# Kernel tuning notes

Measured on AMD Instinct MI355X. Metric: run time of the kernel, lower is better.

## Reference

```python
import jax, jax.numpy as jnp
import numpy as np

C0, C1, C2 = 2000, 10000, 50000  # class cutoffs
D = 1024                          # input_size (hidden dim)
OUT_HEAD = C0 + 2                 # head output: shortlist + 2 cluster logits


def setup_inputs() -> dict:
    key = jax.random.key(0)
    ks = jax.random.split(key, 7)
    s = lambda fan_in: 1.0 / np.sqrt(fan_in)
    x = jax.random.normal(ks[0], (4096, D), dtype=jnp.float32)
    Wh = jax.random.normal(ks[1], (OUT_HEAD, D), dtype=jnp.float32) * s(D)
    bh = jnp.zeros((OUT_HEAD,), dtype=jnp.float32)
    # tail 0: D -> D//4**0 -> (C1-C0)
    W0a = jax.random.normal(ks[2], (D, D), dtype=jnp.float32) * s(D)
    W0b = jax.random.normal(ks[3], (C1 - C0, D), dtype=jnp.float32) * s(D)
    # tail 1: D -> D//4**1 -> (C2-C1)
    W1a = jax.random.normal(ks[4], (D // 4, D), dtype=jnp.float32) * s(D)
    W1b = jax.random.normal(ks[5], (C2 - C1, D // 4), dtype=jnp.float32) * s(D // 4)
    return {"x": x, "Wh": Wh, "bh": bh, "W0a": W0a, "W0b": W0b, "W1a": W1a, "W1b": W1b}


def reference(x, Wh, bh, W0a, W0b, W1a, W1b):
    # head: [B, OUT_HEAD]; log-softmax over shortlist + cluster logits
    lsm_head = jax.nn.log_softmax(x @ Wh.T + bh, axis=-1)
    # tail clusters: capacity-reduction linear, projection, log-softmax within cluster
    lsm_t0 = jax.nn.log_softmax((x @ W0a.T) @ W0b.T, axis=-1)  # [B, C1-C0]
    lsm_t1 = jax.nn.log_softmax((x @ W1a.T) @ W1b.T, axis=-1)  # [B, C2-C1]
    # flat log-probs: cluster log-prob broadcast-added to within-cluster log-probs
    prob = jnp.concatenate([
        lsm_head[:, :C0],
        lsm_head[:, C0:C0 + 1] + lsm_t0,
        lsm_head[:, C0 + 1:C0 + 2] + lsm_t1,
    ], axis=1)  # [B, C2]
    return prob
```

## Files before the change

kernel.cpp:

```cpp
#include <hip/hip_runtime.h>
#include <hip/hip_bf16.h>
#include <math.h>

#define CC0 2000
#define CC1 10000
#define CC2 50000
#define DH  1024
#define BATCH 4096
#define OUT_HEAD (CC0 + 2)

typedef __attribute__((ext_vector_type(4))) float  f32x4;
typedef __attribute__((ext_vector_type(8))) __bf16 bf16x8;
typedef __attribute__((ext_vector_type(8))) short  s16x8;

__device__ __forceinline__ void gload_lds16(const void* g, void* l) {
    __builtin_amdgcn_global_load_lds(
        (const __attribute__((address_space(1))) void*)g,
        (__attribute__((address_space(3))) void*)l, 16, 0, 0);
}

__global__ __launch_bounds__(256) void convert_all_kernel(
    const float4* __restrict__ s0, ushort4* __restrict__ d0, int n0s, int n0d,
    const float4* __restrict__ s1, ushort4* __restrict__ d1, int n1s, int n1d,
    const float4* __restrict__ s2, ushort4* __restrict__ d2, int n2s, int n2d,
    const float4* __restrict__ s3, ushort4* __restrict__ d3, int n3s, int n3d,
    const float4* __restrict__ s4, ushort4* __restrict__ d4, int n4s, int n4d,
    const float4* __restrict__ s5, ushort4* __restrict__ d5, int n5s, int n5d,
    float* __restrict__ rs0, float* __restrict__ rs1)
{
    if (blockIdx.y == 6) {
        int i = blockIdx.x * blockDim.x + threadIdx.x;
        if (i < BATCH) { rs0[i] = 0.f; rs1[i] = 0.f; }
        return;
    }
    const float4* src; ushort4* dst; int ns, nd;
    switch (blockIdx.y) {
        case 0: src = s0; dst = d0; ns = n0s; nd = n0d; break;
        case 1: src = s1; dst = d1; ns = n1s; nd = n1d; break;
        case 2: src = s2; dst = d2; ns = n2s; nd = n2d; break;
        case 3: src = s3; dst = d3; ns = n3s; nd = n3d; break;
        case 4: src = s4; dst = d4; ns = n4s; nd = n4d; break;
        default: src = s5; dst = d5; ns = n5s; nd = n5d; break;
    }
    int i = blockIdx.x * blockDim.x + threadIdx.x;
    const int stride = gridDim.x * blockDim.x;
    for (; i < nd; i += stride) {
        ushort4 o = {0, 0, 0, 0};
        if (i < ns) {
            float4 v = src[i];
            o.x = __builtin_bit_cast(unsigned short, (__bf16)v.x);
            o.y = __builtin_bit_cast(unsigned short, (__bf16)v.y);
            o.z = __builtin_bit_cast(unsigned short, (__bf16)v.z);
            o.w = __builtin_bit_cast(unsigned short, (__bf16)v.w);
        }
        dst[i] = o;
    }
}

__global__ __launch_bounds__(256) void gemm128x3_kernel(
    const ushort* __restrict__ x_bf,
    const ushort* __restrict__ W0a_bf, ushort* __restrict__ h0,
    const ushort* __restrict__ W1a_bf, ushort* __restrict__ h1,
    const ushort* __restrict__ Wh_bf,  float*  __restrict__ headL)
{
    __shared__ ushort As[128 * 64];
    __shared__ ushort Bs[128 * 64];

    const int gb = blockIdx.x;
    const ushort* A = x_bf; const ushort* B; void* C;
    int N, ldC, wmode, nbx, lin;
    const int K = DH;
    if (gb < 256)      { B = W0a_bf; C = h0;    N = DH;       ldC = DH;       wmode = 1; nbx = 8;  lin = gb; }
    else if (gb < 320) { B = W1a_bf; C = h1;    N = 256;      ldC = 256;      wmode = 1; nbx = 2;  lin = gb - 256; }
    else               { B = Wh_bf;  C = headL; N = OUT_HEAD; ldC = OUT_HEAD; wmode = 2; nbx = 16; lin = gb - 320; }

    const int nwg = nbx * 32;
    const int q = nwg >> 3;
    int bid = (lin & 7) * q + (lin >> 3);
    const int bx = bid % nbx;
    const int by = bid / nbx;

    const int t = threadIdx.x;
    const int lane = t & 63;
    const int w = t >> 6;
    const int wr = w >> 1, wc = w & 1;
    const int lr = lane & 15;
    const int lg = lane >> 4;
    const int bm = by * 128;
    const int bn = bx * 128;
    const int lrow = lane >> 3;
    const int lcol = (lane & 7) * 8;

    f32x4 acc[4][4] = {};

    for (int k0 = 0; k0 < K; k0 += 64) {
        #pragma unroll
        for (int i = 0; i < 4; ++i) {
            const int seg = w * 4 + i;
            const int row = seg * 8 + lrow;
            gload_lds16(A + (size_t)(bm + row) * K + k0 + lcol, &As[seg * 512]);
            gload_lds16(B + (size_t)(bn + row) * K + k0 + lcol, &Bs[seg * 512]);
        }
        __syncthreads();
        #pragma unroll
        for (int ks = 0; ks < 2; ++ks) {
            s16x8 af[4], bfr[4];
            #pragma unroll
            for (int m = 0; m < 4; ++m)
                af[m] = *(const s16x8*)&As[(wr * 64 + m * 16 + lr) * 64 + ks * 32 + lg * 8];
            #pragma unroll
            for (int n = 0; n < 4; ++n)
                bfr[n] = *(const s16x8*)&Bs[(wc * 64 + n * 16 + lr) * 64 + ks * 32 + lg * 8];
            #pragma unroll
            for (int m = 0; m < 4; ++m)
                #pragma unroll
                for (int n = 0; n < 4; ++n)
                    acc[m][n] = __builtin_amdgcn_mfma_f32_16x16x32_bf16(
                        __builtin_bit_cast(bf16x8, af[m]),
                        __builtin_bit_cast(bf16x8, bfr[n]), acc[m][n], 0, 0, 0);
        }
        __syncthreads();
    }

    #pragma unroll
    for (int m = 0; m < 4; ++m) {
        #pragma unroll
        for (int r = 0; r < 4; ++r) {
            const int row = bm + wr * 64 + m * 16 + lg * 4 + r;
            #pragma unroll
            for (int n = 0; n < 4; ++n) {
                const int col = bn + wc * 64 + n * 16 + lr;
                float v = acc[m][n][r];
                if (col < N) {
                    if (wmode == 1)
                        ((ushort*)C)[(size_t)row * ldC + col] =
                            __builtin_bit_cast(unsigned short, (__bf16)v);
                    else
                        ((float*)C)[(size_t)row * ldC + col] = v;
                }
            }
        }
    }
}

template <int WMODE, bool SUMEXP>
__global__ __launch_bounds__(512, 1) void gemm256_kernel(
    const ushort* __restrict__ A, const ushort* __restrict__ B,
    void* __restrict__ Cp, int M, int N, int K, int ldC,
    float* __restrict__ rowsum, const float* __restrict__ addv)
{
    __shared__ ushort lds[2][2][256 * 64];

    const int nby = gridDim.y;
    const int nwg = gridDim.x * gridDim.y;
    const int q8 = nwg >> 3;
    int bid = blockIdx.y * gridDim.x + blockIdx.x;
    bid = (bid & 7) * q8 + (bid >> 3);
    const int by = bid % nby;
    const int bx = bid / nby;
    const int bm = by * 256, bn = bx * 256;

    const int t = threadIdx.x;
    const int lane = t & 63;
    const int w = t >> 6;
    const int wr = w >> 2;
    const int wc = w & 3;
    const int lr = lane & 15;
    const int lg = lane >> 4;
    const int xr = (lr & 7) << 4;
    const int c0 = w * 64 + lane;

    f32x4 acc[8][4] = {};
    const int nkt = K / 64;

    auto stage_tile = [&](int ktile, int buf) {
        const int k0 = ktile * 64;
        #pragma unroll
        for (int h = 0; h < 4; ++h) {
            const int r0 = (h >> 1) * 128;
            const int mat = h & 1;
            const ushort* gbase = mat ? B : A;
            const int brow = mat ? bn : bm;
            #pragma unroll
            for (int i = 0; i < 2; ++i) {
                const int c = i * 512 + c0;
                const int rl = c >> 3;
                const int cc = (c & 7) ^ (rl & 7);
                gload_lds16(gbase + (size_t)(brow + r0 + rl) * K + k0 + cc * 8,
                            (char*)&lds[buf][mat][0] + r0 * 128 + (i * 512 + w * 64) * 16);
            }
        }
    };

    stage_tile(0, 0);
    asm volatile("s_waitcnt vmcnt(0)");
    __builtin_amdgcn_s_barrier();
    asm volatile("" ::: "memory");

    for (int tk = 0; tk < nkt; ++tk) {
        const int cur = tk & 1;
        if (tk + 1 < nkt) stage_tile(tk + 1, cur ^ 1);
        const char* baseA = (const char*)&lds[cur][0][0];
        const char* baseB = (const char*)&lds[cur][1][0];

        s16x8 bfr[4][2];
        #pragma unroll
        for (int n_ = 0; n_ < 4; ++n_) {
            const int row = wc * 64 + n_ * 16 + lr;
            #pragma unroll
            for (int ks = 0; ks < 2; ++ks)
                bfr[n_][ks] = *(const s16x8*)(baseB + (row * 128 + ((ks * 64 + lg * 16) ^ xr)));
        }
        #pragma unroll
        for (int mh = 0; mh < 2; ++mh) {
            s16x8 af[4][2];
            #pragma unroll
            for (int m_ = 0; m_ < 4; ++m_) {
                const int row = wr * 128 + (mh * 4 + m_) * 16 + lr;
                #pragma unroll
                for (int ks = 0; ks < 2; ++ks)
                    af[m_][ks] = *(const s16x8*)(baseA + (row * 128 + ((ks * 64 + lg * 16) ^ xr)));
            }
            __builtin_amdgcn_s_setprio(1);
            #pragma unroll
            for (int m_ = 0; m_ < 4; ++m_)
                #pragma unroll
                for (int n_ = 0; n_ < 4; ++n_)
                    #pragma unroll
                    for (int ks = 0; ks < 2; ++ks)
                        acc[mh * 4 + m_][n_] = __builtin_amdgcn_mfma_f32_16x16x32_bf16(
                            __builtin_bit_cast(bf16x8, af[m_][ks]),
                            __builtin_bit_cast(bf16x8, bfr[n_][ks]),
                            acc[mh * 4 + m_][n_], 0, 0, 0);
            __builtin_amdgcn_s_setprio(0);
        }
        asm volatile("s_waitcnt vmcnt(0)" ::: "memory");
        __builtin_amdgcn_s_barrier();
        asm volatile("" ::: "memory");
    }

    #pragma unroll
    for (int m = 0; m < 8; ++m) {
        #pragma unroll
        for (int r = 0; r < 4; ++r) {
            const int row = bm + wr * 128 + m * 16 + lg * 4 + r;
            const float addr_ = (WMODE == 3) ? addv[row] : 0.f;
            float psum = 0.f;
            #pragma unroll
            for (int n = 0; n < 4; ++n) {
                const int col = bn + wc * 64 + n * 16 + lr;
                float v = acc[m][n][r];
                if (col < N) {
                    if (WMODE == 1)
                        ((ushort*)Cp)[(size_t)row * ldC + col] =
                            __builtin_bit_cast(unsigned short, (__bf16)v);
                    else if (WMODE == 3)
                        ((float*)Cp)[(size_t)row * ldC + col] = v + addr_;
                    if (SUMEXP) psum += __expf(v);
                }
            }
            if (SUMEXP) {
                #pragma unroll
                for (int mm = 1; mm < 16; mm <<= 1) psum += __shfl_xor(psum, mm, 64);
                if (lr == 0) atomicAdd(&rowsum[row], psum);
            }
        }
    }
}

__global__ __launch_bounds__(256) void head_lsm_kernel(
    const float* __restrict__ HL, const float* __restrict__ bh,
    float* __restrict__ out, float* __restrict__ s01)
{
    const int row = blockIdx.x;
    const float* L = HL + (size_t)row * OUT_HEAD;
    const int t = threadIdx.x;
    __shared__ float red[4];

    float m = -1e30f;
    for (int i = t; i < OUT_HEAD; i += 256) m = fmaxf(m, L[i] + bh[i]);
    #pragma unroll
    for (int s = 1; s < 64; s <<= 1) m = fmaxf(m, __shfl_xor(m, s, 64));
    if ((t & 63) == 0) red[t >> 6] = m;
    __syncthreads();
    m = fmaxf(fmaxf(red[0], red[1]), fmaxf(red[2], red[3]));

    float sum = 0.f;
    for (int i = t; i < OUT_HEAD; i += 256) sum += __expf(L[i] + bh[i] - m);
    #pragma unroll
    for (int s = 1; s < 64; s <<= 1) sum += __shfl_xor(sum, s, 64);
    __syncthreads();
    if ((t & 63) == 0) red[t >> 6] = sum;
    __syncthreads();
    const float lse = m + logf(red[0] + red[1] + red[2] + red[3]);

    float* orow = out + (size_t)row * CC2;
    for (int i = t; i < CC0; i += 256) orow[i] = L[i] + bh[i] - lse;
    if (t == 0) {
        s01[2 * row + 0] = L[CC0 + 0] + bh[CC0 + 0] - lse;
        s01[2 * row + 1] = L[CC0 + 1] + bh[CC0 + 1] - lse;
    }
}

__global__ __launch_bounds__(256) void prep_add_kernel(
    const float* __restrict__ s01, const float* __restrict__ rs0,
    const float* __restrict__ rs1, float* __restrict__ add0,
    float* __restrict__ add1, int n)
{
    int i = blockIdx.x * blockDim.x + threadIdx.x;
    if (i < n) {
        add0[i] = s01[2 * i + 0] - logf(rs0[i]);
        add1[i] = s01[2 * i + 1] - logf(rs1[i]);
    }
}

__global__ __launch_bounds__(256) void finalize_bf16_kernel(
    const ushort* __restrict__ Lg, int ldL, int ncols8,
    float* __restrict__ outb, const float* __restrict__ addv)
{
    const int row = blockIdx.y;
    const float add = addv[row];
    const int c = blockIdx.x * blockDim.x + threadIdx.x;
    if (c >= ncols8) return;
    s16x8 v = *(const s16x8*)(Lg + (size_t)row * ldL + c * 8);
    float* o = outb + (size_t)row * CC2 + c * 8;
    float4 o0, o1;
    o0.x = __builtin_bit_cast(float, (unsigned)(unsigned short)v[0] << 16) + add;
    o0.y = __builtin_bit_cast(float, (unsigned)(unsigned short)v[1] << 16) + add;
    o0.z = __builtin_bit_cast(float, (unsigned)(unsigned short)v[2] << 16) + add;
    o0.w = __builtin_bit_cast(float, (unsigned)(unsigned short)v[3] << 16) + add;
    o1.x = __builtin_bit_cast(float, (unsigned)(unsigned short)v[4] << 16) + add;
    o1.y = __builtin_bit_cast(float, (unsigned)(unsigned short)v[5] << 16) + add;
    o1.z = __builtin_bit_cast(float, (unsigned)(unsigned short)v[6] << 16) + add;
    o1.w = __builtin_bit_cast(float, (unsigned)(unsigned short)v[7] << 16) + add;
    *(float4*)o = o0;
    *(float4*)(o + 4) = o1;
}

extern "C" void kernel_launch(void* const* d_in, const int* in_sizes, int n_in,
                              void* d_out, int out_size, void* d_ws, size_t ws_size,
                              hipStream_t stream) {
    const float* x   = (const float*)d_in[0];
    const float* Wh  = (const float*)d_in[1];
    const float* bh  = (const float*)d_in[2];
    const float* W0a = (const float*)d_in[3];
    const float* W0b = (const float*)d_in[4];
    const float* W1a = (const float*)d_in[5];
    const float* W1b = (const float*)d_in[6];
    float* out = (float*)d_out;
    char*  ws  = (char*)d_ws;

    const int NH_P  = 2048;
    const int N0_P  = 8192;
    const int N1_P  = 40192;

    size_t off = 0;
    auto alloc = [&](size_t bytes) { size_t o = off; off += (bytes + 255) & ~(size_t)255; return o; };
    ushort* x_bf   = (ushort*)(ws + alloc((size_t)BATCH * DH * 2));
    ushort* Wh_bf  = (ushort*)(ws + alloc((size_t)NH_P * DH * 2));
    ushort* W0a_bf = (ushort*)(ws + alloc((size_t)DH * DH * 2));
    ushort* W0b_bf = (ushort*)(ws + alloc((size_t)N0_P * DH * 2));
    ushort* W1a_bf = (ushort*)(ws + alloc((size_t)256 * DH * 2));
    ushort* W1b_bf = (ushort*)(ws + alloc((size_t)N1_P * 256 * 2));
    ushort* h0_bf  = (ushort*)(ws + alloc((size_t)BATCH * DH * 2));
    ushort* h1_bf  = (ushort*)(ws + alloc((size_t)BATCH * 256 * 2));
    float*  headL  = (float*)(ws + alloc((size_t)BATCH * OUT_HEAD * 4));
    float*  s01    = (float*)(ws + alloc((size_t)BATCH * 2 * 4));
    float*  rs0    = (float*)(ws + alloc((size_t)BATCH * 4));
    float*  rs1    = (float*)(ws + alloc((size_t)BATCH * 4));
    float*  add0   = (float*)(ws + alloc((size_t)BATCH * 4));
    float*  add1   = (float*)(ws + alloc((size_t)BATCH * 4));
    ushort* L0     = (ushort*)(ws + alloc((size_t)BATCH * N0_P * 2));

    convert_all_kernel<<<dim3(1280, 7), 256, 0, stream>>>(
        (const float4*)x,   (ushort4*)x_bf,   BATCH * DH / 4,        BATCH * DH / 4,
        (const float4*)Wh,  (ushort4*)Wh_bf,  OUT_HEAD * DH / 4,     NH_P * DH / 4,
        (const float4*)W0a, (ushort4*)W0a_bf, DH * DH / 4,           DH * DH / 4,
        (const float4*)W0b, (ushort4*)W0b_bf, (CC1 - CC0) * DH / 4,  N0_P * DH / 4,
        (const float4*)W1a, (ushort4*)W1a_bf, 256 * DH / 4,          256 * DH / 4,
        (const float4*)W1b, (ushort4*)W1b_bf, (CC2 - CC1) * 256 / 4, N1_P * 256 / 4,
        rs0, rs1);

    gemm128x3_kernel<<<832, 256, 0, stream>>>(
        x_bf, W0a_bf, h0_bf, W1a_bf, h1_bf, Wh_bf, headL);

    head_lsm_kernel<<<BATCH, 256, 0, stream>>>(headL, bh, out, s01);
    gemm256_kernel<1, true><<<dim3(N0_P / 256, BATCH / 256), 512, 0, stream>>>(
        h0_bf, W0b_bf, L0, BATCH, CC1 - CC0, DH, N0_P, rs0, nullptr);
    gemm256_kernel<0, true><<<dim3(N1_P / 256, BATCH / 256), 512, 0, stream>>>(
        h1_bf, W1b_bf, nullptr, BATCH, CC2 - CC1, 256, 0, rs1, nullptr);
    prep_add_kernel<<<(BATCH + 255) / 256, 256, 0, stream>>>(s01, rs0, rs1, add0, add1, BATCH);
    gemm256_kernel<3, false><<<dim3(N1_P / 256, BATCH / 256), 512, 0, stream>>>(
        h1_bf, W1b_bf, out + CC1, BATCH, CC2 - CC1, 256, CC2, nullptr, add1);
    finalize_bf16_kernel<<<dim3((1000 + 255) / 256, BATCH), 256, 0, stream>>>(
        L0, N0_P, 1000, out + CC0, add0);
}
```

Before: 643.8 us.

## Merge tail GEMMs into one launch and store tail-1 logits instead of recomputing

Both tail projection GEMMs now run in one launch that dispatches on block index. The second cluster's logits are stored as bf16 in a new workspace buffer, so the second GEMM over W1b is no longer run again just to write output. A single finalize kernel then converts both tail buffers to fp32 and adds the per-row offsets. This removes one K=256 GEMM pass and a launch, at the cost of a round trip of about 330 MB through bf16 memory and bf16 rounding of the tail-1 output values.

```diff
diff --git a/kernel.cpp b/kernel.cpp
--- a/kernel.cpp
+++ b/kernel.cpp
@@ -8,6 +8,10 @@
 #define DH  1024
 #define BATCH 4096
 #define OUT_HEAD (CC0 + 2)
+
+#define N0_P 8192
+#define N1_P 40192
+#define NH_P 2048
 
 typedef __attribute__((ext_vector_type(4))) float  f32x4;
 typedef __attribute__((ext_vector_type(8))) __bf16 bf16x8;
@@ -67,7 +71,7 @@
     __shared__ ushort Bs[128 * 64];
 
     const int gb = blockIdx.x;
-    const ushort* A = x_bf; const ushort* B; void* C;
+    const ushort* B; void* C;
     int N, ldC, wmode, nbx, lin;
     const int K = DH;
     if (gb < 256)      { B = W0a_bf; C = h0;    N = DH;       ldC = DH;       wmode = 1; nbx = 8;  lin = gb; }
@@ -98,7 +102,7 @@
         for (int i = 0; i < 4; ++i) {
             const int seg = w * 4 + i;
             const int row = seg * 8 + lrow;
-            gload_lds16(A + (size_t)(bm + row) * K + k0 + lcol, &As[seg * 512]);
+            gload_lds16(x_bf + (size_t)(bm + row) * K + k0 + lcol, &As[seg * 512]);
             gload_lds16(B + (size_t)(bn + row) * K + k0 + lcol, &Bs[seg * 512]);
         }
         __syncthreads();
@@ -123,7 +127,7 @@
     }
 
     #pragma unroll
-    for (int m = 0; m < 4; ++m) {
+    for (int m = 0; m < 4; ++m)
         #pragma unroll
         for (int r = 0; r < 4; ++r) {
             const int row = bm + wr * 64 + m * 16 + lg * 4 + r;
@@ -140,24 +144,27 @@
                 }
             }
         }
-    }
-}
-
-template <int WMODE, bool SUMEXP>
-__global__ __launch_bounds__(512, 1) void gemm256_kernel(
-    const ushort* __restrict__ A, const ushort* __restrict__ B,
-    void* __restrict__ Cp, int M, int N, int K, int ldC,
-    float* __restrict__ rowsum, const float* __restrict__ addv)
+}
+
+__global__ __launch_bounds__(512, 1) void tails256_kernel(
+    const ushort* __restrict__ h0, const ushort* __restrict__ W0b,
+    ushort* __restrict__ L0, float* __restrict__ rs0,
+    const ushort* __restrict__ h1, const ushort* __restrict__ W1b,
+    ushort* __restrict__ L1, float* __restrict__ rs1)
 {
     __shared__ ushort lds[2][2][256 * 64];
 
-    const int nby = gridDim.y;
-    const int nwg = gridDim.x * gridDim.y;
+    const int gb = blockIdx.x;
+    const ushort *A, *B; ushort* C; float* rsum;
+    int K, N, nbx, ldC, lin;
+    if (gb < 512) { A = h0; B = W0b; C = L0; rsum = rs0; K = DH;  N = CC1 - CC0; nbx = N0_P / 256; ldC = N0_P; lin = gb; }
+    else          { A = h1; B = W1b; C = L1; rsum = rs1; K = 256; N = CC2 - CC1; nbx = N1_P / 256; ldC = N1_P; lin = gb - 512; }
+
+    const int nwg = nbx * 16;
     const int q8 = nwg >> 3;
-    int bid = blockIdx.y * gridDim.x + blockIdx.x;
-    bid = (bid & 7) * q8 + (bid >> 3);
-    const int by = bid % nby;
-    const int bx = bid / nby;
+    int bid = (lin & 7) * q8 + (lin >> 3);
+    const int by = bid % 16;
+    const int bx = bid / 16;
     const int bm = by * 256, bn = bx * 256;
 
     const int t = threadIdx.x;
@@ -244,26 +251,20 @@
         #pragma unroll
         for (int r = 0; r < 4; ++r) {
             const int row = bm + wr * 128 + m * 16 + lg * 4 + r;
-            const float addr_ = (WMODE == 3) ? addv[row] : 0.f;
             float psum = 0.f;
             #pragma unroll
             for (int n = 0; n < 4; ++n) {
                 const int col = bn + wc * 64 + n * 16 + lr;
                 float v = acc[m][n][r];
                 if (col < N) {
-                    if (WMODE == 1)
-                        ((ushort*)Cp)[(size_t)row * ldC + col] =
-                            __builtin_bit_cast(unsigned short, (__bf16)v);
-                    else if (WMODE == 3)
-                        ((float*)Cp)[(size_t)row * ldC + col] = v + addr_;
-                    if (SUMEXP) psum += __expf(v);
+                    C[(size_t)row * ldC + col] =
+                        __builtin_bit_cast(unsigned short, (__bf16)v);
+                    psum += __expf(v);
                 }
             }
-            if (SUMEXP) {
-                #pragma unroll
-                for (int mm = 1; mm < 16; mm <<= 1) psum += __shfl_xor(psum, mm, 64);
-                if (lr == 0) atomicAdd(&rowsum[row], psum);
-            }
+            #pragma unroll
+            for (int mm = 1; mm < 16; mm <<= 1) psum += __shfl_xor(psum, mm, 64);
+            if (lr == 0) atomicAdd(&rsum[row], psum);
         }
     }
 }
@@ -314,16 +315,25 @@
     }
 }
 
-__global__ __launch_bounds__(256) void finalize_bf16_kernel(
-    const ushort* __restrict__ Lg, int ldL, int ncols8,
-    float* __restrict__ outb, const float* __restrict__ addv)
+__global__ __launch_bounds__(256) void finalize_all_kernel(
+    const ushort* __restrict__ L0, const ushort* __restrict__ L1,
+    const float* __restrict__ add0, const float* __restrict__ add1,
+    float* __restrict__ out)
 {
     const int row = blockIdx.y;
-    const float add = addv[row];
     const int c = blockIdx.x * blockDim.x + threadIdx.x;
-    if (c >= ncols8) return;
-    s16x8 v = *(const s16x8*)(Lg + (size_t)row * ldL + c * 8);
-    float* o = outb + (size_t)row * CC2 + c * 8;
+    const ushort* src; float* dst; float add;
+    if (c < 1000) {
+        src = L0 + (size_t)row * N0_P + c * 8;
+        dst = out + (size_t)row * CC2 + CC0 + c * 8;
+        add = add0[row];
+    } else if (c < 6000) {
+        const int c1 = c - 1000;
+        src = L1 + (size_t)row * N1_P + c1 * 8;
+        dst = out + (size_t)row * CC2 + CC1 + c1 * 8;
+        add = add1[row];
+    } else return;
+    s16x8 v = *(const s16x8*)src;
     float4 o0, o1;
     o0.x = __builtin_bit_cast(float, (unsigned)(unsigned short)v[0] << 16) + add;
     o0.y = __builtin_bit_cast(float, (unsigned)(unsigned short)v[1] << 16) + add;
@@ -333,8 +343,8 @@
     o1.y = __builtin_bit_cast(float, (unsigned)(unsigned short)v[5] << 16) + add;
     o1.z = __builtin_bit_cast(float, (unsigned)(unsigned short)v[6] << 16) + add;
     o1.w = __builtin_bit_cast(float, (unsigned)(unsigned short)v[7] << 16) + add;
-    *(float4*)o = o0;
-    *(float4*)(o + 4) = o1;
+    *(float4*)dst = o0;
+    *(float4*)(dst + 4) = o1;
 }
 
 extern "C" void kernel_launch(void* const* d_in, const int* in_sizes, int n_in,
@@ -349,10 +359,6 @@
     const float* W1b = (const float*)d_in[6];
     float* out = (float*)d_out;
     char*  ws  = (char*)d_ws;
-
-    const int NH_P  = 2048;
-    const int N0_P  = 8192;
-    const int N1_P  = 40192;
 
     size_t off = 0;
     auto alloc = [&](size_t bytes) { size_t o = off; off += (bytes + 255) & ~(size_t)255; return o; };
@@ -371,6 +377,7 @@
     float*  add0   = (float*)(ws + alloc((size_t)BATCH * 4));
     float*  add1   = (float*)(ws + alloc((size_t)BATCH * 4));
     ushort* L0     = (ushort*)(ws + alloc((size_t)BATCH * N0_P * 2));
+    ushort* L1     = (ushort*)(ws + alloc((size_t)BATCH * N1_P * 2));
 
     convert_all_kernel<<<dim3(1280, 7), 256, 0, stream>>>(
         (const float4*)x,   (ushort4*)x_bf,   BATCH * DH / 4,        BATCH * DH / 4,
@@ -385,13 +392,11 @@
         x_bf, W0a_bf, h0_bf, W1a_bf, h1_bf, Wh_bf, headL);
 
     head_lsm_kernel<<<BATCH, 256, 0, stream>>>(headL, bh, out, s01);
-    gemm256_kernel<1, true><<<dim3(N0_P / 256, BATCH / 256), 512, 0, stream>>>(
-        h0_bf, W0b_bf, L0, BATCH, CC1 - CC0, DH, N0_P, rs0, nullptr);
-    gemm256_kernel<0, true><<<dim3(N1_P / 256, BATCH / 256), 512, 0, stream>>>(
-        h1_bf, W1b_bf, nullptr, BATCH, CC2 - CC1, 256, 0, rs1, nullptr);
+
+    tails256_kernel<<<512 + (N1_P / 256) * 16, 512, 0, stream>>>(
+        h0_bf, W0b_bf, L0, rs0, h1_bf, W1b_bf, L1, rs1);
+
     prep_add_kernel<<<(BATCH + 255) / 256, 256, 0, stream>>>(s01, rs0, rs1, add0, add1, BATCH);
-    gemm256_kernel<3, false><<<dim3(N1_P / 256, BATCH / 256), 512, 0, stream>>>(
-        h1_bf, W1b_bf, out + CC1, BATCH, CC2 - CC1, 256, CC2, nullptr, add1);
-    finalize_bf16_kernel<<<dim3((1000 + 255) / 256, BATCH), 256, 0, stream>>>(
-        L0, N0_P, 1000, out + CC0, add0);
-}
+
+    finalize_all_kernel<<<dim3(24, BATCH), 256, 0, stream>>>(L0, L1, add0, add1, out);
+}
```

Measured after the change: 616.9 us. 1.04x faster.
